# Optimization experiments

Measured on AMD Instinct MI355X. Metric: run time of the kernel, lower is better.

## Reference

```python
import jax, jax.numpy as jnp
import numpy as np

N_USER, N_MOVIE, E, H, L = 100000, 20000, 1000000, 64, 2
NEG_SLOPE = 0.2  # PyG GATv2Conv default negative_slope


def _rand_edges(k, n_src, n_dst, e):
    k1, k2 = jax.random.split(k)
    src = jax.random.randint(k1, (e,), 0, n_src, dtype=jnp.int32)
    dst = jax.random.randint(k2, (e,), 0, n_dst, dtype=jnp.int32)
    # ensure no src==dst index collisions so PyG's remove_self_loops is a no-op
    dst = jnp.where(dst == src, (dst + 1) % n_dst, dst)
    return jnp.stack([src, dst])


def setup_inputs() -> dict:
    key = jax.random.key(0)
    ks = jax.random.split(key, 8)
    return {
        "x_user": jax.random.normal(ks[0], (N_USER, H), jnp.float32),
        "x_movie": jax.random.normal(ks[1], (N_MOVIE, H), jnp.float32),
        "edge_u2m": _rand_edges(ks[2], N_USER, N_MOVIE, E),
        "edge_m2u": _rand_edges(ks[3], N_MOVIE, N_USER, E),
        # params stacked as [layer, edge_type, ...]; edge_type 0 = user->movie, 1 = movie->user
        "Wl": jax.random.normal(ks[4], (L, 2, H, H), jnp.float32) / np.sqrt(H).astype(np.float32),
        "bl": jnp.zeros((L, 2, H), jnp.float32),
        "Wr": jax.random.normal(ks[5], (L, 2, H, H), jnp.float32) / np.sqrt(H).astype(np.float32),
        "br": jnp.zeros((L, 2, H), jnp.float32),
        "att": jax.random.normal(ks[6], (L, 2, H), jnp.float32) / np.sqrt(H).astype(np.float32),
        "bias": jnp.zeros((L, 2, H), jnp.float32),
    }


def _segment_softmax(scores, seg, n):
    # numerically-stable softmax over variable-degree dst neighborhoods (PyG softmax)
    m = jax.ops.segment_max(scores, seg, num_segments=n)
    ex = jnp.exp(scores - m[seg])
    s = jax.ops.segment_sum(ex, seg, num_segments=n)
    return ex / (s[seg] + 1e-16)


def _gatv2(x_src, x_dst, edge, Wl, bl, Wr, br, att, bias):
    n_src, n_dst = x_src.shape[0], x_dst.shape[0]
    xl = x_src @ Wl + bl  # [N_src, H]
    xr = x_dst @ Wr + br  # [N_dst, H]
    n_loop = min(n_src, n_dst)  # PyG adds self loops with num_nodes = min(N_src, N_dst)
    loop = jnp.arange(n_loop, dtype=edge.dtype)
    src = jnp.concatenate([edge[0], loop])
    dst = jnp.concatenate([edge[1], loop])
    e = jax.nn.leaky_relu(xl[src] + xr[dst], NEG_SLOPE)  # [E', H] gathered per edge
    score = e @ att  # [E']
    alpha = _segment_softmax(score, dst, n_dst)
    out = jax.ops.segment_sum(xl[src] * alpha[:, None], dst, num_segments=n_dst)
    return out + bias


def reference(x_user, x_movie, edge_u2m, edge_m2u, Wl, bl, Wr, br, att, bias):
    for l in range(L):
        new_movie = _gatv2(x_user, x_movie, edge_u2m,
                           Wl[l, 0], bl[l, 0], Wr[l, 0], br[l, 0], att[l, 0], bias[l, 0])
        new_user = _gatv2(x_movie, x_user, edge_m2u,
                          Wl[l, 1], bl[l, 1], Wr[l, 1], br[l, 1], att[l, 1], bias[l, 1])
        x_movie = jax.nn.selu(new_movie)
        x_user = jax.nn.selu(new_user)
    return x_user, x_movie
```

## Files before the change

### kernel.cpp

```cpp
#include <hip/hip_runtime.h>
#include <hip/hip_fp16.h>
#include <cstdint>

#define H 64
#define EPR 16
#define NB 120

__device__ __forceinline__ float selu_f(float x) {
  const float sc = 1.0507009873554805f;
  const float al = 1.6732632423543772f;
  return x > 0.f ? sc * x : sc * al * (expf(x) - 1.f);
}

__global__ __launch_bounds__(128) void gemm64_quad(
    const float* __restrict__ Au, const float* __restrict__ Am,
    const float* __restrict__ W0u, const float* __restrict__ b0u,
    const float* __restrict__ W1u, const float* __restrict__ b1u,
    const float* __restrict__ W0m, const float* __restrict__ b0m,
    const float* __restrict__ W1m, const float* __restrict__ b1m,
    __half* __restrict__ C0u, float* __restrict__ C1u,
    __half* __restrict__ C0m, float* __restrict__ C1m,
    int Nu, int Nm, int su, int sm) {
  __shared__ float Ws[64 * 64];
  __shared__ float bs[64];

  const int b = blockIdx.x;
  const float *A, *W, *bias; __half* Ch = nullptr; float* Cf = nullptr;
  int N, blk; bool half_out;
  if (b < su)            { A = Au; W = W0u; bias = b0u; Ch = C0u; N = Nu; blk = b;            half_out = true; }
  else if (b < 2 * su)   { A = Au; W = W1u; bias = b1u; Cf = C1u; N = Nu; blk = b - su;       half_out = false; }
  else if (b < 2*su+sm)  { A = Am; W = W0m; bias = b0m; Ch = C0m; N = Nm; blk = b - 2*su;     half_out = true; }
  else                   { A = Am; W = W1m; bias = b1m; Cf = C1m; N = Nm; blk = b - 2*su - sm; half_out = false; }

  const int tid = threadIdx.x;
  for (int i = tid; i < 1024; i += 128) ((float4*)Ws)[i] = ((const float4*)W)[i];
  if (tid < 64) bs[tid] = bias[tid];
  __syncthreads();

  const int g = tid & 3;
  const int tr = tid >> 2;
  const int row0 = blk * 128;

  float acc[4][16];
#pragma unroll
  for (int i = 0; i < 4; ++i)
#pragma unroll
    for (int j = 0; j < 16; ++j) acc[i][j] = bs[g * 16 + j];

  int rows[4]; int ar[4]; bool rok[4];
#pragma unroll
  for (int i = 0; i < 4; ++i) {
    rows[i] = row0 + tr + 32 * i;
    rok[i] = rows[i] < N;
    ar[i] = rok[i] ? rows[i] : (N - 1);
  }

  for (int kt = 0; kt < 4; ++kt) {
    float av[4][16];
#pragma unroll
    for (int i = 0; i < 4; ++i) {
      const float4* ap = (const float4*)(A + (size_t)ar[i] * H + kt * 16);
#pragma unroll
      for (int c = 0; c < 4; ++c) {
        float4 v = ap[c];
        av[i][4 * c + 0] = v.x; av[i][4 * c + 1] = v.y;
        av[i][4 * c + 2] = v.z; av[i][4 * c + 3] = v.w;
      }
    }
#pragma unroll
    for (int kk = 0; kk < 16; ++kk) {
      const int k = kt * 16 + kk;
      const float4* wr = (const float4*)&Ws[k * 64 + g * 16];
      float w[16];
#pragma unroll
      for (int c = 0; c < 4; ++c) {
        float4 t = wr[c];
        w[4 * c + 0] = t.x; w[4 * c + 1] = t.y;
        w[4 * c + 2] = t.z; w[4 * c + 3] = t.w;
      }
#pragma unroll
      for (int i = 0; i < 4; ++i) {
        float a = av[i][kk];
#pragma unroll
        for (int j = 0; j < 16; ++j) acc[i][j] = fmaf(a, w[j], acc[i][j]);
      }
    }
  }

#pragma unroll
  for (int i = 0; i < 4; ++i) {
    if (!rok[i]) continue;
    if (half_out) {
      unsigned pu[8];
#pragma unroll
      for (int j2 = 0; j2 < 8; ++j2) {
        __half2 t = __floats2half2_rn(acc[i][2 * j2], acc[i][2 * j2 + 1]);
        pu[j2] = *(unsigned*)&t;
      }
      uint4* c0 = (uint4*)(Ch + (size_t)rows[i] * H + g * 16);
      c0[0] = make_uint4(pu[0], pu[1], pu[2], pu[3]);
      c0[1] = make_uint4(pu[4], pu[5], pu[6], pu[7]);
    } else {
      float4* c1 = (float4*)(Cf + (size_t)rows[i] * H + g * 16);
#pragma unroll
      for (int c = 0; c < 4; ++c)
        c1[c] = make_float4(acc[i][4 * c + 0], acc[i][4 * c + 1],
                            acc[i][4 * c + 2], acc[i][4 * c + 3]);
    }
  }
}

__global__ __launch_bounds__(256) void bucket_hist(
    const int* __restrict__ ed1, int E1r, int n1e, int sh1, int B1, int* __restrict__ mat1,
    const int* __restrict__ ed2, int E2r, int n2e, int sh2, int B2, int* __restrict__ mat2) {
  __shared__ int hist[640];
  int b = blockIdx.x;
  const int* ed; int Er, ne, sh, Bn, blk; int* mat;
  if (b < NB) { ed = ed1; Er = E1r; ne = n1e; sh = sh1; Bn = B1; mat = mat1; blk = b; }
  else { ed = ed2; Er = E2r; ne = n2e; sh = sh2; Bn = B2; mat = mat2; blk = b - NB; }
  for (int i = threadIdx.x; i < Bn; i += 256) hist[i] = 0;
  __syncthreads();
  int chunk = (ne + NB - 1) / NB;
  int lo = blk * chunk, hi = lo + chunk;
  if (hi > ne) hi = ne;
  for (int e = lo + threadIdx.x; e < hi; e += 256) {
    int d = (e < Er) ? ed[e] : (e - Er);
    atomicAdd(&hist[d >> sh], 1);
  }
  __syncthreads();
  for (int i = threadIdx.x; i < Bn; i += 256) mat[(size_t)i * NB + blk] = hist[i];
}

__global__ __launch_bounds__(256) void scan_partial2(
    const int* __restrict__ cnt1, int n1, int* __restrict__ psum1, int* __restrict__ bsum1,
    const int* __restrict__ cnt2, int n2, int* __restrict__ psum2, int* __restrict__ bsum2,
    int split) {
  __shared__ int sh[256];
  int b = blockIdx.x;
  const int* cnt; int n; int* psum; int* bsum; int lb;
  if (b < split) { cnt = cnt1; n = n1; psum = psum1; bsum = bsum1; lb = b; }
  else { cnt = cnt2; n = n2; psum = psum2; bsum = bsum2; lb = b - split; }
  int i = lb * 256 + threadIdx.x;
  int tid = threadIdx.x;
  sh[tid] = (i < n) ? cnt[i] : 0;
  __syncthreads();
  for (int off = 1; off < 256; off <<= 1) {
    int t = (tid >= off) ? sh[tid - off] : 0;
    __syncthreads();
    if (tid >= off) sh[tid] += t;
    __syncthreads();
  }
  if (i < n) psum[i] = sh[tid];
  if (tid == 255) bsum[lb] = sh[255];
}

__global__ __launch_bounds__(256) void scan_bsums2(
    int* __restrict__ bsum1, int nb1, int* __restrict__ bsum2, int nb2) {
  __shared__ int sh[256];
  const int tid = threadIdx.x;
  for (int which = 0; which < 2; ++which) {
    int* bsum = which ? bsum2 : bsum1;
    int nb = which ? nb2 : nb1;
    int run = 0;
    for (int start = 0; start < nb; start += 256) {
      int i = start + tid;
      int v = (i < nb) ? bsum[i] : 0;
      __syncthreads();
      sh[tid] = v;
      __syncthreads();
      for (int off = 1; off < 256; off <<= 1) {
        int t = (tid >= off) ? sh[tid - off] : 0;
        __syncthreads();
        if (tid >= off) sh[tid] += t;
        __syncthreads();
      }
      if (i < nb) bsum[i] = run + sh[tid] - v;
      run += sh[255];
      __syncthreads();
    }
  }
}

__global__ __launch_bounds__(256) void finalize_excl2(
    const int* __restrict__ cnt1, const int* __restrict__ psum1,
    const int* __restrict__ bsum1, int n1, int* __restrict__ excl1,
    const int* __restrict__ cnt2, const int* __restrict__ psum2,
    const int* __restrict__ bsum2, int n2, int* __restrict__ excl2, int split) {
  int b = blockIdx.x;
  const int *cnt, *psum, *bsum; int n; int* excl; int lb;
  if (b < split) { cnt = cnt1; psum = psum1; bsum = bsum1; n = n1; excl = excl1; lb = b; }
  else { cnt = cnt2; psum = psum2; bsum = bsum2; n = n2; excl = excl2; lb = b - split; }
  int i = lb * 256 + threadIdx.x;
  if (i >= n) return;
  excl[i] = psum[i] + bsum[lb] - cnt[i];
}

__global__ __launch_bounds__(256) void bucket_part(
    const int* __restrict__ es1, const int* __restrict__ ed1, int E1r, int n1e,
    int sh1, int B1, const int* __restrict__ excl1, unsigned* __restrict__ part1,
    const int* __restrict__ es2, const int* __restrict__ ed2, int E2r, int n2e,
    int sh2, int B2, const int* __restrict__ excl2, unsigned* __restrict__ part2) {
  __shared__ int cur[640];
  int b = blockIdx.x;
  const int *es, *ed, *excl; int Er, ne, sh, Bn, blk; unsigned* part;
  if (b < NB) { es = es1; ed = ed1; Er = E1r; ne = n1e; sh = sh1; Bn = B1; excl = excl1; part = part1; blk = b; }
  else { es = es2; ed = ed2; Er = E2r; ne = n2e; sh = sh2; Bn = B2; excl = excl2; part = part2; blk = b - NB; }
  for (int i = threadIdx.x; i < Bn; i += 256) cur[i] = excl[(size_t)i * NB + blk];
  __syncthreads();
  int chunk = (ne + NB - 1) / NB;
  int lo = blk * chunk, hi = lo + chunk;
  if (hi > ne) hi = ne;
  const unsigned lmask = (1u << sh) - 1u;
  for (int e = lo + threadIdx.x; e < hi; e += 256) {
    int s, d;
    if (e < Er) { s = es[e]; d = ed[e]; } else { s = e - Er; d = s; }
    int bkt = d >> sh;
    int pos = atomicAdd(&cur[bkt], 1);
    part[pos] = (((unsigned)d & lmask) << 18) | (unsigned)s;
  }
}

__global__ __launch_bounds__(256) void bucket_sort(
    const unsigned* __restrict__ part1, const int* __restrict__ excl1,
    int n1e, int sh1, int B1, int nd1, int* __restrict__ rp1, int* __restrict__ csr1,
    const unsigned* __restrict__ part2, const int* __restrict__ excl2,
    int n2e, int sh2, int B2, int nd2, int* __restrict__ rp2, int* __restrict__ csr2) {
  __shared__ int cnt_s[256];
  __shared__ int scan_s[256];
  int b = blockIdx.x;
  const unsigned* part; const int* excl; int ne, sh, Bn, nd, bkt; int *rp, *csr;
  if (b < B1) { part = part1; excl = excl1; ne = n1e; sh = sh1; Bn = B1; nd = nd1; rp = rp1; csr = csr1; bkt = b; }
  else { part = part2; excl = excl2; ne = n2e; sh = sh2; Bn = B2; nd = nd2; rp = rp2; csr = csr2; bkt = b - B1; }
  const int tid = threadIdx.x;
  const int dbase = bkt << sh;
  const int R = 1 << sh;
  int rcap = nd - dbase;
  if (rcap > R) rcap = R;
  const int base = excl[(size_t)bkt * NB];
  const int endv = (bkt == Bn - 1) ? ne : excl[(size_t)(bkt + 1) * NB];

  cnt_s[tid] = 0;
  __syncthreads();
  for (int i = base + tid; i < endv; i += 256)
    atomicAdd(&cnt_s[part[i] >> 18], 1);
  __syncthreads();
  int c = cnt_s[tid];
  scan_s[tid] = c;
  __syncthreads();
  for (int off = 1; off < 256; off <<= 1) {
    int t = (tid >= off) ? scan_s[tid - off] : 0;
    __syncthreads();
    if (tid >= off) scan_s[tid] += t;
    __syncthreads();
  }
  if (tid < rcap) rp[dbase + tid + 1] = base + scan_s[tid];
  cnt_s[tid] = base + scan_s[tid] - c;
  if (tid == 0 && bkt == 0) rp[0] = 0;
  __syncthreads();
  for (int i = base + tid; i < endv; i += 256) {
    unsigned p = part[i];
    int dl = p >> 18;
    int pos = atomicAdd(&cnt_s[dl], 1);
    csr[pos] = (int)(p & 0x3FFFFu);
  }
}

__global__ __launch_bounds__(256) void gat_dst2(
    const int* __restrict__ rp1, const int* __restrict__ csr1,
    const __half* __restrict__ xl1, const float* __restrict__ xr1,
    const float* __restrict__ att1, const float* __restrict__ bias1,
    float* __restrict__ out1, int nd1,
    const int* __restrict__ rp2, const int* __restrict__ csr2,
    const __half* __restrict__ xl2, const float* __restrict__ xr2,
    const float* __restrict__ att2, const float* __restrict__ bias2,
    float* __restrict__ out2, int nd2, int split) {
  __shared__ __align__(16) float tile[4][EPR * 64];

  const int b = blockIdx.x;
  const int* rp; const int* csr; const __half* xl; const float *xr, *att, *bias;
  float* out; int nd, d0;
  if (b < split) {
    rp = rp1; csr = csr1; xl = xl1; xr = xr1; att = att1; bias = bias1;
    out = out1; nd = nd1; d0 = b * 4;
  } else {
    rp = rp2; csr = csr2; xl = xl2; xr = xr2; att = att2; bias = bias2;
    out = out2; nd = nd2; d0 = (b - split) * 4;
  }
  const int w = threadIdx.x >> 6;
  const int d = d0 + w;
  if (d >= nd) return;
  const int h = threadIdx.x & 63;
  const unsigned h2 = (unsigned)h * 2u;
  const char* xlb = (const char*)xl;
  float* tl = tile[w];

  const float xr_h = xr[(size_t)d * H + h];
  const float a = att[h];
  const float a06 = 0.6f * a, a04 = 0.4f * a;
  const float bias_h = bias[h];
  const int sbeg = __builtin_amdgcn_readfirstlane(rp[d]);
  const int send = __builtin_amdgcn_readfirstlane(rp[d + 1]);

  const int r = h & 15;
  const int q = h >> 4;
  const int pr = (q << 2) ^ r;

  float o;

  if (send - sbeg <= EPR) {
    const int cnt = send - sbeg;
    const int* csw = csr + sbeg;
    float v[EPR];
#pragma unroll
    for (int qq = 0; qq < EPR / 4; ++qq) {
      if (qq * 4 < cnt) {
#pragma unroll
        for (int i = 0; i < 4; ++i) {
          const int k = qq * 4 + i;
          int j = k < cnt ? k : cnt - 1;
          unsigned src = (unsigned)csw[j];
          v[k] = __half2float(*(const __half*)(xlb + ((src << 7) | h2)));
        }
      }
    }
#pragma unroll
    for (int qq = 0; qq < EPR / 4; ++qq) {
      if (qq * 4 < cnt) {
#pragma unroll
        for (int i = 0; i < 4; ++i) {
          const int k = qq * 4 + i;
          float p = v[k] + xr_h;
          tl[(k << 6) | (h ^ (k << 2))] = fmaf(p, a06, fabsf(p) * a04);
        }
      }
    }
    const float4* t4 = (const float4*)tl;
    float t0 = 0.f, t1 = 0.f, t2 = 0.f, t3 = 0.f;
#pragma unroll
    for (int c = 0; c < 4; ++c) {
      float4 q4 = t4[(r << 4) | (pr ^ c)];
      t0 += q4.x; t1 += q4.y; t2 += q4.z; t3 += q4.w;
    }
    float t = (t0 + t1) + (t2 + t3);
    t += __shfl_xor(t, 16, 64);
    t += __shfl_xor(t, 32, 64);
    t = (r < cnt) ? t : -3.0e38f;

    float M = t;
#pragma unroll
    for (int mk = 1; mk <= 8; mk <<= 1) M = fmaxf(M, __shfl_xor(M, mk, 64));
    float e = __expf(t - M);
    float S = e;
#pragma unroll
    for (int mk = 1; mk <= 8; mk <<= 1) S += __shfl_xor(S, mk, 64);
    if (h < 16) tl[h] = e;

    float P = 0.f;
#pragma unroll
    for (int qq = 0; qq < EPR / 4; ++qq) {
      if (qq * 4 < cnt) {
        float4 w4 = ((const float4*)tl)[qq];
        P += w4.x * v[qq * 4 + 0];
        P += w4.y * v[qq * 4 + 1];
        P += w4.z * v[qq * 4 + 2];
        P += w4.w * v[qq * 4 + 3];
      }
    }
    o = P / (S + 1e-16f) + bias_h;
  } else {
    float m = -3.0e38f, s = 0.f, acc = 0.f;
    int base = sbeg;
    float v[EPR], v2[EPR];

    {
      const int* csw = csr + base;
#pragma unroll
      for (int k = 0; k < EPR; ++k) {
        unsigned src = (unsigned)csw[k];
        v[k] = __half2float(*(const __half*)(xlb + ((src << 7) | h2)));
      }
    }

    auto round = [&](float (&vc)[EPR], float (&vp)[EPR]) -> bool {
      int cnt = send - base;
      if (cnt > EPR) cnt = EPR;
#pragma unroll
      for (int qq = 0; qq < EPR / 4; ++qq) {
        if (qq * 4 < cnt) {
#pragma unroll
          for (int i = 0; i < 4; ++i) {
            const int k = qq * 4 + i;
            float p = vc[k] + xr_h;
            tl[(k << 6) | (h ^ (k << 2))] = fmaf(p, a06, fabsf(p) * a04);
          }
        }
      }
      const int nbase = base + EPR;
      int ncnt = send - nbase;
      const bool have_next = ncnt > 0;
      if (ncnt > EPR) ncnt = EPR;
      if (have_next) {
        const int* csn = csr + nbase;
#pragma unroll
        for (int qq = 0; qq < EPR / 4; ++qq) {
          if (qq * 4 < ncnt) {
#pragma unroll
            for (int i = 0; i < 4; ++i) {
              const int k = qq * 4 + i;
              int j = k < ncnt ? k : ncnt - 1;
              unsigned src = (unsigned)csn[j];
              vp[k] = __half2float(*(const __half*)(xlb + ((src << 7) | h2)));
            }
          }
        }
      }
      const float4* t4 = (const float4*)tl;
      float t0 = 0.f, t1 = 0.f, t2 = 0.f, t3 = 0.f;
#pragma unroll
      for (int c = 0; c < 4; ++c) {
        float4 q4 = t4[(r << 4) | (pr ^ c)];
        t0 += q4.x; t1 += q4.y; t2 += q4.z; t3 += q4.w;
      }
      float t = (t0 + t1) + (t2 + t3);
      t += __shfl_xor(t, 16, 64);
      t += __shfl_xor(t, 32, 64);
      t = (r < cnt) ? t : -3.0e38f;

      float M = t;
#pragma unroll
      for (int mk = 1; mk <= 8; mk <<= 1) M = fmaxf(M, __shfl_xor(M, mk, 64));
      float e = __expf(t - M);
      float S = e;
#pragma unroll
      for (int mk = 1; mk <= 8; mk <<= 1) S += __shfl_xor(S, mk, 64);
      if (h < 16) tl[h] = e;

      float nm = fmaxf(m, M);
      float a_old = __expf(m - nm);
      float a_new = __expf(M - nm);
      float P = 0.f;
#pragma unroll
      for (int qq = 0; qq < EPR / 4; ++qq) {
        if (qq * 4 < cnt) {
          float4 w4 = ((const float4*)tl)[qq];
          P += w4.x * vc[qq * 4 + 0];
          P += w4.y * vc[qq * 4 + 1];
          P += w4.z * vc[qq * 4 + 2];
          P += w4.w * vc[qq * 4 + 3];
        }
      }
      s = s * a_old + S * a_new;
      acc = acc * a_old + P * a_new;
      m = nm;
      base = nbase;
      return have_next;
    };

    for (;;) {
      if (!round(v, v2)) break;
      if (!round(v2, v)) break;
    }
    o = acc / (s + 1e-16f) + bias_h;
  }

  out[(size_t)d * H + h] = selu_f(o);
}

extern "C" void kernel_launch(void* const* d_in, const int* in_sizes, int n_in,
                              void* d_out, int out_size, void* d_ws, size_t ws_size,
                              hipStream_t stream) {
  const float* x_user = (const float*)d_in[0];
  const float* x_movie = (const float*)d_in[1];
  const int* e_u2m = (const int*)d_in[2];
  const int* e_m2u = (const int*)d_in[3];
  const float* Wl = (const float*)d_in[4];
  const float* bl = (const float*)d_in[5];
  const float* Wr = (const float*)d_in[6];
  const float* br = (const float*)d_in[7];
  const float* att = (const float*)d_in[8];
  const float* bias = (const float*)d_in[9];

  const int n_user = in_sizes[0] / H;
  const int n_movie = in_sizes[1] / H;
  const int E1 = in_sizes[2] / 2;
  const int E2 = in_sizes[3] / 2;
  const int n_loop = n_user < n_movie ? n_user : n_movie;
  const int nE1 = E1 + n_loop;
  const int nE2 = E2 + n_loop;

  const int SHM = 5, SHU = 8;
  const int Bm = (n_movie + (1 << SHM) - 1) >> SHM;
  const int Bu = (n_user + (1 << SHU) - 1) >> SHU;
  const int nmatM = Bm * NB, nmatU = Bu * NB;
  const int nbm = (nmatM + 255) / 256, nbu = (nmatU + 255) / 256;

  float* ws = (float*)d_ws;
  size_t o = 0;
  __half* xl_u2m = (__half*)(ws + o); o += (size_t)n_user * H / 2;
  __half* xl_m2u = (__half*)(ws + o); o += (size_t)n_movie * H / 2;
  float* xr_u2m = ws + o; o += (size_t)n_movie * H;
  float* xr_m2u = ws + o; o += (size_t)n_user * H;

  int* matM  = (int*)(ws + o); o += nmatM;
  int* psumM = (int*)(ws + o); o += nmatM;
  int* exclM = (int*)(ws + o); o += nmatM;
  int* matU  = (int*)(ws + o); o += nmatU;
  int* psumU = (int*)(ws + o); o += nmatU;
  int* exclU = (int*)(ws + o); o += nmatU;
  int* bsumM = (int*)(ws + o); o += 1024;
  int* bsumU = (int*)(ws + o); o += 1024;
  unsigned* partM = (unsigned*)(ws + o); o += nE1;
  unsigned* partU = (unsigned*)(ws + o); o += nE2;
  int* csr1 = (int*)(ws + o); o += nE1;
  int* csr2 = (int*)(ws + o); o += nE2;
  int* rp1  = (int*)(ws + o); o += n_movie + 1;
  int* rp2  = (int*)(ws + o); o += n_user + 1;

  float* out_u = (float*)d_out;
  float* out_m = out_u + (size_t)n_user * H;

  const int su = (n_user + 127) / 128;
  const int sm = (n_movie + 127) / 128;
  const int split1 = (n_movie + 3) / 4;
  const int split2 = (n_user + 3) / 4;

  bucket_hist<<<2 * NB, 256, 0, stream>>>(
      e_u2m + E1, E1, nE1, SHM, Bm, matM,
      e_m2u + E2, E2, nE2, SHU, Bu, matU);
  scan_partial2<<<nbm + nbu, 256, 0, stream>>>(
      matM, nmatM, psumM, bsumM, matU, nmatU, psumU, bsumU, nbm);
  scan_bsums2<<<1, 256, 0, stream>>>(bsumM, nbm, bsumU, nbu);
  finalize_excl2<<<nbm + nbu, 256, 0, stream>>>(
      matM, psumM, bsumM, nmatM, exclM,
      matU, psumU, bsumU, nmatU, exclU, nbm);
  bucket_part<<<2 * NB, 256, 0, stream>>>(
      e_u2m, e_u2m + E1, E1, nE1, SHM, Bm, exclM, partM,
      e_m2u, e_m2u + E2, E2, nE2, SHU, Bu, exclU, partU);
  bucket_sort<<<Bm + Bu, 256, 0, stream>>>(
      partM, exclM, nE1, SHM, Bm, n_movie, rp1, csr1,
      partU, exclU, nE2, SHU, Bu, n_user, rp2, csr2);

  for (int l = 0; l < 2; ++l) {
    const float* cu = (l == 0) ? x_user : out_u;
    const float* cm = (l == 0) ? x_movie : out_m;
    const int p0 = l * 2 + 0;
    const int p1 = l * 2 + 1;

    gemm64_quad<<<2 * (su + sm), 128, 0, stream>>>(
        cu, cm,
        Wl + (size_t)p0 * H * H, bl + (size_t)p0 * H,
        Wr + (size_t)p1 * H * H, br + (size_t)p1 * H,
        Wl + (size_t)p1 * H * H, bl + (size_t)p1 * H,
        Wr + (size_t)p0 * H * H, br + (size_t)p0 * H,
        xl_u2m, xr_m2u, xl_m2u, xr_u2m,
        n_user, n_movie, su, sm);

    gat_dst2<<<split1 + split2, 256, 0, stream>>>(
        rp1, csr1, xl_u2m, xr_u2m, att + (size_t)p0 * H, bias + (size_t)p0 * H,
        out_m, n_movie,
        rp2, csr2, xl_m2u, xr_m2u, att + (size_t)p1 * H, bias + (size_t)p1 * H,
        out_u, n_user, split1);
  }
}
```

Baseline: 469.0 us.

## Stage A tile in shared memory and double GEMM block threads

Result: faster. 428.0 us (-8.7%).

```diff
diff --git a/kernel.cpp b/kernel.cpp
--- a/kernel.cpp
+++ b/kernel.cpp
@@ -12,7 +12,7 @@
   return x > 0.f ? sc * x : sc * al * (expf(x) - 1.f);
 }
 
-__global__ __launch_bounds__(128) void gemm64_quad(
+__global__ __launch_bounds__(256) void gemm64_split(
     const float* __restrict__ Au, const float* __restrict__ Am,
     const float* __restrict__ W0u, const float* __restrict__ b0u,
     const float* __restrict__ W1u, const float* __restrict__ b1u,
@@ -22,90 +22,78 @@
     __half* __restrict__ C0m, float* __restrict__ C1m,
     int Nu, int Nm, int su, int sm) {
   __shared__ float Ws[64 * 64];
+  __shared__ float As[128][65];
   __shared__ float bs[64];
 
   const int b = blockIdx.x;
   const float *A, *W, *bias; __half* Ch = nullptr; float* Cf = nullptr;
   int N, blk; bool half_out;
-  if (b < su)            { A = Au; W = W0u; bias = b0u; Ch = C0u; N = Nu; blk = b;            half_out = true; }
-  else if (b < 2 * su)   { A = Au; W = W1u; bias = b1u; Cf = C1u; N = Nu; blk = b - su;       half_out = false; }
-  else if (b < 2*su+sm)  { A = Am; W = W0m; bias = b0m; Ch = C0m; N = Nm; blk = b - 2*su;     half_out = true; }
-  else                   { A = Am; W = W1m; bias = b1m; Cf = C1m; N = Nm; blk = b - 2*su - sm; half_out = false; }
+  if (b < su)             { A = Au; W = W0u; bias = b0u; Ch = C0u; N = Nu; blk = b;             half_out = true; }
+  else if (b < 2 * su)    { A = Au; W = W1u; bias = b1u; Cf = C1u; N = Nu; blk = b - su;        half_out = false; }
+  else if (b < 2*su + sm) { A = Am; W = W0m; bias = b0m; Ch = C0m; N = Nm; blk = b - 2*su;      half_out = true; }
+  else                    { A = Am; W = W1m; bias = b1m; Cf = C1m; N = Nm; blk = b - 2*su - sm; half_out = false; }
 
   const int tid = threadIdx.x;
-  for (int i = tid; i < 1024; i += 128) ((float4*)Ws)[i] = ((const float4*)W)[i];
+  for (int i = tid; i < 1024; i += 256) ((float4*)Ws)[i] = ((const float4*)W)[i];
   if (tid < 64) bs[tid] = bias[tid];
+
+  const int row0 = blk * 128;
+  for (int i = tid; i < 2048; i += 256) {
+    int r = i >> 4, c4 = i & 15;
+    int row = row0 + r;
+    float4 v = make_float4(0.f, 0.f, 0.f, 0.f);
+    if (row < N) v = ((const float4*)(A + (size_t)row * H))[c4];
+    As[r][c4 * 4 + 0] = v.x;
+    As[r][c4 * 4 + 1] = v.y;
+    As[r][c4 * 4 + 2] = v.z;
+    As[r][c4 * 4 + 3] = v.w;
+  }
   __syncthreads();
 
   const int g = tid & 3;
   const int tr = tid >> 2;
-  const int row0 = blk * 128;
-
-  float acc[4][16];
-#pragma unroll
-  for (int i = 0; i < 4; ++i)
-#pragma unroll
-    for (int j = 0; j < 16; ++j) acc[i][j] = bs[g * 16 + j];
-
-  int rows[4]; int ar[4]; bool rok[4];
-#pragma unroll
-  for (int i = 0; i < 4; ++i) {
-    rows[i] = row0 + tr + 32 * i;
-    rok[i] = rows[i] < N;
-    ar[i] = rok[i] ? rows[i] : (N - 1);
-  }
-
-  for (int kt = 0; kt < 4; ++kt) {
-    float av[4][16];
-#pragma unroll
-    for (int i = 0; i < 4; ++i) {
-      const float4* ap = (const float4*)(A + (size_t)ar[i] * H + kt * 16);
-#pragma unroll
-      for (int c = 0; c < 4; ++c) {
-        float4 v = ap[c];
-        av[i][4 * c + 0] = v.x; av[i][4 * c + 1] = v.y;
-        av[i][4 * c + 2] = v.z; av[i][4 * c + 3] = v.w;
-      }
-    }
-#pragma unroll
-    for (int kk = 0; kk < 16; ++kk) {
-      const int k = kt * 16 + kk;
-      const float4* wr = (const float4*)&Ws[k * 64 + g * 16];
-      float w[16];
-#pragma unroll
-      for (int c = 0; c < 4; ++c) {
-        float4 t = wr[c];
-        w[4 * c + 0] = t.x; w[4 * c + 1] = t.y;
-        w[4 * c + 2] = t.z; w[4 * c + 3] = t.w;
-      }
-#pragma unroll
-      for (int i = 0; i < 4; ++i) {
-        float a = av[i][kk];
-#pragma unroll
-        for (int j = 0; j < 16; ++j) acc[i][j] = fmaf(a, w[j], acc[i][j]);
-      }
-    }
-  }
-
-#pragma unroll
-  for (int i = 0; i < 4; ++i) {
-    if (!rok[i]) continue;
+  float acc0[16], acc1[16];
+#pragma unroll
+  for (int j = 0; j < 16; ++j) { acc0[j] = bs[g * 16 + j]; acc1[j] = bs[g * 16 + j]; }
+
+  for (int k = 0; k < 64; ++k) {
+    float a0 = As[tr][k];
+    float a1 = As[tr + 64][k];
+    const float4* wr = (const float4*)&Ws[k * 64 + g * 16];
+#pragma unroll
+    for (int c = 0; c < 4; ++c) {
+      float4 w = wr[c];
+      acc0[4 * c + 0] = fmaf(a0, w.x, acc0[4 * c + 0]);
+      acc0[4 * c + 1] = fmaf(a0, w.y, acc0[4 * c + 1]);
+      acc0[4 * c + 2] = fmaf(a0, w.z, acc0[4 * c + 2]);
+      acc0[4 * c + 3] = fmaf(a0, w.w, acc0[4 * c + 3]);
+      acc1[4 * c + 0] = fmaf(a1, w.x, acc1[4 * c + 0]);
+      acc1[4 * c + 1] = fmaf(a1, w.y, acc1[4 * c + 1]);
+      acc1[4 * c + 2] = fmaf(a1, w.z, acc1[4 * c + 2]);
+      acc1[4 * c + 3] = fmaf(a1, w.w, acc1[4 * c + 3]);
+    }
+  }
+
+#pragma unroll
+  for (int half = 0; half < 2; ++half) {
+    const int row = row0 + tr + 64 * half;
+    if (row >= N) continue;
+    const float* acc = half ? acc1 : acc0;
     if (half_out) {
       unsigned pu[8];
 #pragma unroll
       for (int j2 = 0; j2 < 8; ++j2) {
-        __half2 t = __floats2half2_rn(acc[i][2 * j2], acc[i][2 * j2 + 1]);
+        __half2 t = __floats2half2_rn(acc[2 * j2], acc[2 * j2 + 1]);
         pu[j2] = *(unsigned*)&t;
       }
-      uint4* c0 = (uint4*)(Ch + (size_t)rows[i] * H + g * 16);
+      uint4* c0 = (uint4*)(Ch + (size_t)row * H + g * 16);
       c0[0] = make_uint4(pu[0], pu[1], pu[2], pu[3]);
       c0[1] = make_uint4(pu[4], pu[5], pu[6], pu[7]);
     } else {
-      float4* c1 = (float4*)(Cf + (size_t)rows[i] * H + g * 16);
+      float4* c1 = (float4*)(Cf + (size_t)row * H + g * 16);
 #pragma unroll
       for (int c = 0; c < 4; ++c)
-        c1[c] = make_float4(acc[i][4 * c + 0], acc[i][4 * c + 1],
-                            acc[i][4 * c + 2], acc[i][4 * c + 3]);
+        c1[c] = make_float4(acc[4 * c + 0], acc[4 * c + 1], acc[4 * c + 2], acc[4 * c + 3]);
     }
   }
 }
@@ -546,7 +534,7 @@
     const int p0 = l * 2 + 0;
     const int p1 = l * 2 + 1;
 
-    gemm64_quad<<<2 * (su + sm), 128, 0, stream>>>(
+    gemm64_split<<<2 * (su + sm), 256, 0, stream>>>(
         cu, cm,
         Wl + (size_t)p0 * H * H, bl + (size_t)p0 * H,
         Wr + (size_t)p1 * H * H, br + (size_t)p1 * H,
```
